# Kernel optimization log

Hardware: AMD Instinct MI355X
Metric: run time of the kernel (lower is better)

The kernel has to match this reference:

```python
import jax, jax.numpy as jnp
import numpy as np

B, S, D, H = 4, 2048, 1024, 16
HD = D // H
BITS = 8
LEVELS = 2 ** BITS - 1          # number of negative log2 levels
SCALING = 32.0 / 16.0           # lora alpha / rank for 8-bit adapter
NEG_INF = -1e9


def log_fake_quant(x, reduce_axes):
    """Per-channel log-domain fake quantization with straight-through estimator.
    Scale = per-channel max-abs; magnitudes snapped to power-of-two fractions of scale."""
    s = jnp.maximum(jnp.max(jnp.abs(x), axis=reduce_axes, keepdims=True), 1e-8)
    ratio = jnp.clip(jnp.abs(x) / s, 2.0 ** (-LEVELS), 1.0)
    e = jnp.round(jnp.log2(ratio))                      # in [-LEVELS, 0]
    q = jnp.sign(x) * s * jnp.exp2(e)
    return x + jax.lax.stop_gradient(q - x)             # STE


def cpt_linear(x, W, b, lA, lB):
    """CPTLinear: fake-quantized activation/weight GEMM + bias + LoRA on the fp input."""
    xq = log_fake_quant(x, tuple(range(x.ndim - 1)))     # per last-dim channel
    Wq = log_fake_quant(W, (1,))                         # per output row (channel_dim=0)
    out = xq @ Wq.T + b
    return out + (x @ lA @ lB) * SCALING


def setup_inputs() -> dict:
    key = jax.random.key(0)
    ks = jax.random.split(key, 8)
    causal = jnp.tril(jnp.ones((S, S), dtype=bool))
    mask = jnp.where(causal, 0.0, NEG_INF).astype(jnp.float32)[None, None]  # [1,1,S,S]
    return {
        "hidden_states": jax.random.normal(ks[0], (B, S, D), jnp.float32),
        "attention_mask": mask,
        "W_attn": jax.random.normal(ks[1], (3 * D, D), jnp.float32) * 0.02,
        "b_attn": jnp.zeros((3 * D,), jnp.float32),
        "lA_attn": jax.random.normal(ks[2], (D, 16), jnp.float32) * 0.01,
        "lB_attn": jax.random.normal(ks[3], (16, 3 * D), jnp.float32) * 0.01,
        "W_proj": jax.random.normal(ks[4], (D, D), jnp.float32) * 0.02,
        "b_proj": jnp.zeros((D,), jnp.float32),
        "lA_proj": jax.random.normal(ks[5], (D, 16), jnp.float32) * 0.01,
        "lB_proj": jax.random.normal(ks[6], (16, D), jnp.float32) * 0.01,
    }


def reference(hidden_states, attention_mask, W_attn, b_attn, lA_attn, lB_attn,
              W_proj, b_proj, lA_proj, lB_proj):
    qkv = cpt_linear(hidden_states, W_attn, b_attn, lA_attn, lB_attn)  # [B,S,3D]
    q, k, v = jnp.split(qkv, 3, axis=-1)

    def to_heads(t):
        return t.reshape(B, S, H, HD).transpose(0, 2, 1, 3)            # [B,H,S,HD]

    q, k, v = to_heads(q), to_heads(k), to_heads(v)
    scores = jnp.einsum("bhqd,bhkd->bhqk", q, k) / np.float32(np.sqrt(HD))
    scores = scores + attention_mask
    attn = jax.nn.softmax(scores, axis=-1)                             # dropout: eval mode (identity)
    out = jnp.einsum("bhqk,bhkd->bhqd", attn, v)
    out = out.transpose(0, 2, 1, 3).reshape(B, S, D)
    return cpt_linear(out, W_proj, b_proj, lA_proj, lB_proj)
```

## Files before the change

kernel.cpp:

```cpp
#include <hip/hip_runtime.h>

#define SS 2048
#define DD 1024
#define DQKV 3072
#define KP 1088
#define NT64 17
#define MTOT 8192
#define QKSZ ((size_t)MTOT * DD)
#define SCL 0.18033688011112042f

typedef unsigned short us;
typedef __attribute__((ext_vector_type(8))) short bf16x8;
typedef __attribute__((ext_vector_type(4))) float f32x4;
typedef __attribute__((ext_vector_type(4))) unsigned u32x4;

#define WAITVM(N) asm volatile("s_waitcnt vmcnt(" #N ")" ::: "memory")
#define WAITLGKM0 asm volatile("s_waitcnt lgkmcnt(0)" ::: "memory")

__device__ __forceinline__ us f2bf(float f) {
    unsigned u = __float_as_uint(f);
    return (us)((u + 0x7fffu + ((u >> 16) & 1u)) >> 16);
}
__device__ __forceinline__ float bf2f(us h) { return __uint_as_float(((unsigned)h) << 16); }
__device__ __forceinline__ void split2(float q, us& h, us& l) {
    h = f2bf(q); l = f2bf(q - bf2f(h));
}
__device__ __forceinline__ unsigned cvtpk(float lo, float hi) {
    unsigned r;
    asm("v_cvt_pk_bf16_f32 %0, %1, %2" : "=v"(r) : "v"(lo), "v"(hi));
    return r;
}

__device__ __forceinline__ int logq_e(float ax, float s) {
    int e = 0;
    if (ax < s) {
        int ex;
        float m = frexpf(ax / s, &ex);
        int k = (m >= 0.70710678f) ? ex : ex - 1;
        double ax2 = (double)ax * (double)ax;
        double s2 = (double)s * (double)s;
        if (ax2 >= ldexp(s2, 2 * k + 1)) k += 1;
        else if (ax2 < ldexp(s2, 2 * k - 1)) k -= 1;
        if (k > 0) k = 0;
        e = (k < -255) ? -255 : k;
    }
    return e;
}
__device__ __forceinline__ float logq_exact(float x, float s) {
    float ax = fabsf(x);
    if (ax == 0.f) return copysignf(0.f, x);
    return copysignf(ldexpf(s, logq_e(ax, s)), x);
}

__device__ __forceinline__ void gll16(const void* g, void* l) {
    __builtin_amdgcn_global_load_lds(
        (const __attribute__((address_space(1))) void*)g,
        (__attribute__((address_space(3))) void*)l, 16, 0, 0);
}


__global__ void k_colmax(const float* __restrict__ x, unsigned* __restrict__ smax) {
    int c = blockIdx.x * 256 + threadIdx.x;
    int r0 = blockIdx.y * 128;
    float m = 0.f;
    for (int r = 0; r < 128; ++r) m = fmaxf(m, fabsf(x[(size_t)(r0 + r) * DD + c]));
    atomicMax(smax + c, __float_as_uint(m));
}

__global__ __launch_bounds__(256) void k_quant_lora(const float* __restrict__ x,
                                                    const unsigned* __restrict__ smax,
                                                    const float* __restrict__ lA,
                                                    us* __restrict__ xq) {
    __shared__ float red[4][16];
    int m = blockIdx.x, tx = threadIdx.x;
    int lane = tx & 63, w = tx >> 6;
    float4 xv = ((const float4*)(x + (size_t)m * DD))[tx];
    int c = tx * 4;
    float vv[4] = {xv.x, xv.y, xv.z, xv.w};
    ushort4 qh;
    us* ph = (us*)&qh;
#pragma unroll
    for (int j = 0; j < 4; ++j) {
        float s = fmaxf(__uint_as_float(smax[c + j]), 1e-8f);
        float sh = bf2f(f2bf(s));
        float ax = fabsf(vv[j]);
        if (ax == 0.f) ph[j] = (us)((__float_as_uint(vv[j]) >> 16) & 0x8000u);
        else ph[j] = f2bf(copysignf(ldexpf(sh, logq_e(ax, s)), vv[j]));
    }
    *(ushort4*)(xq + (size_t)m * KP + c) = qh;
    float acc[16];
#pragma unroll
    for (int r = 0; r < 16; ++r) acc[r] = 0.f;
#pragma unroll
    for (int j = 0; j < 4; ++j) {
        float xs = vv[j];
        const float4* lr = (const float4*)(lA + (size_t)(c + j) * 16);
        float4 a0 = lr[0], a1 = lr[1], a2 = lr[2], a3 = lr[3];
        acc[0] += xs * a0.x; acc[1] += xs * a0.y; acc[2] += xs * a0.z; acc[3] += xs * a0.w;
        acc[4] += xs * a1.x; acc[5] += xs * a1.y; acc[6] += xs * a1.z; acc[7] += xs * a1.w;
        acc[8] += xs * a2.x; acc[9] += xs * a2.y; acc[10] += xs * a2.z; acc[11] += xs * a2.w;
        acc[12] += xs * a3.x; acc[13] += xs * a3.y; acc[14] += xs * a3.z; acc[15] += xs * a3.w;
    }
#pragma unroll
    for (int msk = 1; msk < 64; msk <<= 1)
#pragma unroll
        for (int r = 0; r < 16; ++r) acc[r] += __shfl_xor(acc[r], msk);
    if (lane == 0)
#pragma unroll
        for (int r = 0; r < 16; ++r) red[w][r] = acc[r];
    __syncthreads();
    if (tx < 16) {
        float v = 2.0f * (red[0][tx] + red[1][tx] + red[2][tx] + red[3][tx]);
        us h, l; split2(v, h, l);
        xq[(size_t)m * KP + 1024 + tx] = h;
        xq[(size_t)m * KP + 1040 + tx] = l;
    } else if (tx == 16) {
        xq[(size_t)m * KP + 1056] = 0x3F80;
    } else if (tx < 48) {
        xq[(size_t)m * KP + 1040 + tx] = 0;
    }
}

__global__ __launch_bounds__(256) void k_quant_w(const float* __restrict__ W, const float* __restrict__ lB,
                                                 const float* __restrict__ bias,
                                                 const unsigned* __restrict__ smax,
                                                 us* __restrict__ wh, us* __restrict__ wl, int Nn) {
    __shared__ float red[4];
    int n = blockIdx.x, tx = threadIdx.x;
    int lane = tx & 63, w = tx >> 6;
    float4 wv = ((const float4*)(W + (size_t)n * DD))[tx];
    float m4 = fmaxf(fmaxf(fabsf(wv.x), fabsf(wv.y)), fmaxf(fabsf(wv.z), fabsf(wv.w)));
#pragma unroll
    for (int msk = 1; msk < 64; msk <<= 1) m4 = fmaxf(m4, __shfl_xor(m4, msk));
    if (lane == 0) red[w] = m4;
    __syncthreads();
    float t = fmaxf(fmaxf(fmaxf(red[0], red[1]), fmaxf(red[2], red[3])), 1e-8f);
    float vv[4] = {wv.x, wv.y, wv.z, wv.w};
    int c = tx * 4;
    ushort4 qh, ql;
    us* ph = (us*)&qh; us* pl = (us*)&ql;
#pragma unroll
    for (int j = 0; j < 4; ++j) {
        float s = fmaxf(__uint_as_float(smax[c + j]), 1e-8f);
        float sh = bf2f(f2bf(s));
        float rho = (s - sh) / sh;
        float q = logq_exact(vv[j], t);
        float wp = q + q * rho;
        split2(wp, ph[j], pl[j]);
    }
    *(ushort4*)(wh + (size_t)n * KP + c) = qh;
    *(ushort4*)(wl + (size_t)n * KP + c) = ql;
    if (tx < 64) {
        us h = 0, l = 0;
        if (tx < 32) { int r = tx & 15; split2(lB[(size_t)r * Nn + n], h, l); }
        else if (tx == 32) split2(bias[n], h, l);
        wh[(size_t)n * KP + 1024 + tx] = h;
        wl[(size_t)n * KP + 1024 + tx] = l;
    }
}


template <int MODE>
__global__ __launch_bounds__(512, 2) void k_gemm(const us* __restrict__ Aq_,
                                                 const us* __restrict__ Bh_, const us* __restrict__ Bl_,
                                                 float* __restrict__ C, int Nn,
                                                 us* __restrict__ Khg, us* __restrict__ Klg,
                                                 float* __restrict__ vbuf) {
    __shared__ us LA[2][16384];
    __shared__ us LBh[2][8192];
    __shared__ us LBl[2][8192];
    int tid = threadIdx.x;
    int bn = blockIdx.x, bm = blockIdx.y;
    int lane = tid & 63, w = tid >> 6;
    int wm = w >> 2, wn = w & 3;
    int l15 = lane & 15, l4 = lane >> 4;
    int srow = tid >> 3;
    int gsrc = ((tid & 7) ^ (srow & 7)) * 8;
    const us* aP  = Aq_ + (size_t)(bm * 256 + srow) * KP + gsrc;
    const us* bhP = Bh_ + (size_t)(bn * 128 + srow) * KP + gsrc;
    const us* blP = Bl_ + (size_t)(bn * 128 + srow) * KP + gsrc;
    f32x4 zero4 = {0.f, 0.f, 0.f, 0.f};
    f32x4 acc[8][2];
#pragma unroll
    for (int i = 0; i < 8; ++i) { acc[i][0] = zero4; acc[i][1] = zero4; }

#define GSTAGE(buf, kt)                                               \
    do {                                                              \
        int k0_ = (kt) * 64;                                          \
        gll16(aP + k0_,                    &LA[(buf)][0]     + tid * 8); \
        gll16(aP + (size_t)64  * KP + k0_, &LA[(buf)][4096]  + tid * 8); \
        gll16(aP + (size_t)128 * KP + k0_, &LA[(buf)][8192]  + tid * 8); \
        gll16(aP + (size_t)192 * KP + k0_, &LA[(buf)][12288] + tid * 8); \
        gll16(bhP + k0_,                   &LBh[(buf)][0]    + tid * 8); \
        gll16(bhP + (size_t)64 * KP + k0_, &LBh[(buf)][4096] + tid * 8); \
        gll16(blP + k0_,                   &LBl[(buf)][0]    + tid * 8); \
        gll16(blP + (size_t)64 * KP + k0_, &LBl[(buf)][4096] + tid * 8); \
    } while (0)

    GSTAGE(0, 0);
    GSTAGE(1, 1);
    WAITVM(8);
    __builtin_amdgcn_s_barrier();
    __builtin_amdgcn_sched_barrier(0);

    int gsw0 = ((l4)     ^ (l15 & 7)) * 8;
    int gsw1 = ((4 + l4) ^ (l15 & 7)) * 8;
    int cur = 0;
    for (int kt = 0; kt < NT64; ++kt) {
        const us* A0  = &LA[cur][0];
        const us* Bh0 = &LBh[cur][0];
        const us* Bl0 = &LBl[cur][0];
        bf16x8 a0[8], b0h[2], b0l[2];
#pragma unroll
        for (int i = 0; i < 8; ++i)
            a0[i] = *(const bf16x8*)(A0 + (wm * 128 + i * 16 + l15) * 64 + gsw0);
#pragma unroll
        for (int i = 0; i < 2; ++i) {
            b0h[i] = *(const bf16x8*)(Bh0 + (wn * 32 + i * 16 + l15) * 64 + gsw0);
            b0l[i] = *(const bf16x8*)(Bl0 + (wn * 32 + i * 16 + l15) * 64 + gsw0);
        }
        __builtin_amdgcn_s_setprio(1);
#pragma unroll
        for (int mi = 0; mi < 8; ++mi)
#pragma unroll
            for (int ni = 0; ni < 2; ++ni) {
                acc[mi][ni] = __builtin_amdgcn_mfma_f32_16x16x32_bf16(a0[mi], b0h[ni], acc[mi][ni], 0, 0, 0);
                acc[mi][ni] = __builtin_amdgcn_mfma_f32_16x16x32_bf16(a0[mi], b0l[ni], acc[mi][ni], 0, 0, 0);
            }
        __builtin_amdgcn_s_setprio(0);
        bf16x8 a1[8], b1h[2], b1l[2];
#pragma unroll
        for (int i = 0; i < 8; ++i)
            a1[i] = *(const bf16x8*)(A0 + (wm * 128 + i * 16 + l15) * 64 + gsw1);
#pragma unroll
        for (int i = 0; i < 2; ++i) {
            b1h[i] = *(const bf16x8*)(Bh0 + (wn * 32 + i * 16 + l15) * 64 + gsw1);
            b1l[i] = *(const bf16x8*)(Bl0 + (wn * 32 + i * 16 + l15) * 64 + gsw1);
        }
        WAITLGKM0;
        __builtin_amdgcn_sched_barrier(0);
        __builtin_amdgcn_s_barrier();
        __builtin_amdgcn_sched_barrier(0);
        if (kt + 2 < NT64) GSTAGE(cur, kt + 2);
        __builtin_amdgcn_s_setprio(1);
#pragma unroll
        for (int mi = 0; mi < 8; ++mi)
#pragma unroll
            for (int ni = 0; ni < 2; ++ni) {
                acc[mi][ni] = __builtin_amdgcn_mfma_f32_16x16x32_bf16(a1[mi], b1h[ni], acc[mi][ni], 0, 0, 0);
                acc[mi][ni] = __builtin_amdgcn_mfma_f32_16x16x32_bf16(a1[mi], b1l[ni], acc[mi][ni], 0, 0, 0);
            }
        __builtin_amdgcn_s_setprio(0);
        if (kt + 2 < NT64) { WAITVM(8); } else { WAITVM(0); }
        __builtin_amdgcn_s_barrier();
        __builtin_amdgcn_sched_barrier(0);
        cur ^= 1;
    }
#undef GSTAGE

    int plane = bn >> 3;
#pragma unroll
    for (int mi = 0; mi < 8; ++mi) {
#pragma unroll
        for (int ni = 0; ni < 2; ++ni) {
            int ncol = bn * 128 + wn * 32 + ni * 16 + l15;
            size_t mbase = (size_t)bm * 256 + wm * 128 + mi * 16 + l4 * 4;
#pragma unroll
            for (int rr = 0; rr < 4; ++rr) {
                float v = acc[mi][ni][rr];
                size_t m = mbase + rr;
                if (MODE == 0) {
                    C[m * (size_t)Nn + ncol] = v;
                } else {
                    int cc = ncol & 1023;
                    if (plane == 0) {
                        C[m * DD + cc] = v;
                    } else if (plane == 2) {
                        vbuf[m * DD + cc] = v;
                    } else {
                        us hh, ll; split2(v * SCL, hh, ll);
                        size_t d = ((size_t)((m >> 11) * 16 + (cc >> 6)) * SS + (m & 2047)) * 64 + (cc & 63);
                        Khg[d] = hh; Klg[d] = ll;
                    }
                }
            }
        }
    }
}


__global__ __launch_bounds__(256) void k_transpose_v(const float* __restrict__ vbuf,
                                                     us* __restrict__ vth, us* __restrict__ vtl) {
    __shared__ us th[64][72], tl[64][72];
    int st = blockIdx.x, bh = blockIdx.y;
    int bb = bh >> 4, h = bh & 15;
    int s0 = st * 64, tid = threadIdx.x;
    int sl = tid >> 2, c0 = (tid & 3) * 16;
    const float* src = vbuf + (size_t)(bb * SS + s0 + sl) * DD + h * 64 + c0;
#pragma unroll
    for (int j4 = 0; j4 < 4; ++j4) {
        float4 v = *(const float4*)(src + j4 * 4);
        float vv[4] = {v.x, v.y, v.z, v.w};
#pragma unroll
        for (int j = 0; j < 4; ++j) {
            us hh, ll; split2(vv[j], hh, ll);
            th[c0 + j4 * 4 + j][sl] = hh;
            tl[c0 + j4 * 4 + j][sl] = ll;
        }
    }
    __syncthreads();
#pragma unroll
    for (int p = 0; p < 2; ++p) {
        int gidx = p * 256 + tid;
        int hd = gidx >> 3, g = gidx & 7;
        int base = (g >> 2) * 32 + (g & 3) * 4;
        ushort4 a, b2, c, d2;
        a.x = th[hd][base];      a.y = th[hd][base + 1];  a.z = th[hd][base + 2];  a.w = th[hd][base + 3];
        b2.x = th[hd][base + 16]; b2.y = th[hd][base + 17]; b2.z = th[hd][base + 18]; b2.w = th[hd][base + 19];
        c.x = tl[hd][base];      c.y = tl[hd][base + 1];  c.z = tl[hd][base + 2];  c.w = tl[hd][base + 3];
        d2.x = tl[hd][base + 16]; d2.y = tl[hd][base + 17]; d2.z = tl[hd][base + 18]; d2.w = tl[hd][base + 19];
        size_t dof = ((size_t)bh * 64 + hd) * SS + s0 + g * 8;
        *(ushort4*)(vth + dof) = a;  *(ushort4*)(vth + dof + 4) = b2;
        *(ushort4*)(vtl + dof) = c;  *(ushort4*)(vtl + dof + 4) = d2;
    }
}


__global__ __launch_bounds__(512, 2) void k_attn(float* qo,
                                                 const us* __restrict__ Khg, const us* __restrict__ Klg,
                                                 const us* __restrict__ vth, const us* __restrict__ vtl) {
    __shared__ us L[2][16384];
    int bh = blockIdx.x;
    int qt = (int)(gridDim.y - 1) - blockIdx.y;
    int b = bh >> 4, h = bh & 15;
    int q0 = qt * 128;
    int tid = threadIdx.x, w = tid >> 6, lane = tid & 63;
    int l15 = lane & 15, l4 = lane >> 4;
    int qw = q0 + w * 16;
    int swz = l15 & 7;

    bf16x8 qh[2], ql[2];
#pragma unroll
    for (int hf = 0; hf < 2; ++hf) {
        const float* qp = qo + (size_t)(b * SS + qw + l15) * DD + h * 64 + hf * 32 + l4 * 8;
        float4 a = *(const float4*)qp;
        float4 c = *(const float4*)(qp + 4);
        float vv[8] = {a.x, a.y, a.z, a.w, c.x, c.y, c.z, c.w};
        bf16x8 hq, lq;
#pragma unroll
        for (int j = 0; j < 8; ++j) {
            us hh = f2bf(vv[j]);
            hq[j] = (short)hh;
            lq[j] = (short)f2bf(vv[j] - bf2f(hh));
        }
        qh[hf] = hq; ql[hf] = lq;
    }

    f32x4 zero4 = {0.f, 0.f, 0.f, 0.f};
    f32x4 of[4];
#pragma unroll
    for (int j = 0; j < 4; ++j) of[j] = zero4;
    float mrow = -1e30f, lrowp = 0.f;

    int r0 = tid >> 3, sl0 = (tid & 7) ^ (r0 & 7);
    int koff0 = (bh * SS + r0) * 64 + sl0 * 8;
    int voff0 = (bh * 64 + r0) * SS + sl0 * 8;

    int ntiles = qt * 2 + 2;

#define STAGE(buf, tt)                                           \
    do {                                                         \
        int kv_ = (tt) * 64;                                     \
        us* D_ = &L[(buf)][0];                                   \
        int kadd_ = kv_ << 6;                                    \
        gll16(Khg + koff0 + kadd_, D_ + tid * 8);                \
        gll16(Klg + koff0 + kadd_, D_ + 4096 + tid * 8);         \
        gll16(vth + voff0 + kv_, D_ + 8192 + tid * 8);           \
        gll16(vtl + voff0 + kv_, D_ + 12288 + tid * 8);          \
    } while (0)

    STAGE(0, 0);
    STAGE(1, 1);
    int cur = 0;

    for (int t = 0; t < ntiles; ++t) {
        int kv0 = t * 64;
        if (t + 1 < ntiles) { WAITVM(4); } else { WAITVM(0); }
        __builtin_amdgcn_s_barrier();

        if (kv0 <= qw + 15) {
            const us* Lc = &L[cur][0];

            f32x4 sf[4];
#pragma unroll
            for (int i = 0; i < 4; ++i) sf[i] = zero4;
            __builtin_amdgcn_s_setprio(1);
#pragma unroll
            for (int kb = 0; kb < 4; ++kb) {
                int rbase = (kb * 16 + l15) * 64;
#pragma unroll
                for (int hf = 0; hf < 2; ++hf) {
                    int off = rbase + (((hf * 4 + l4) ^ swz) * 8);
                    bf16x8 kh = *(const bf16x8*)(Lc + off);
                    bf16x8 kl = *(const bf16x8*)(Lc + 4096 + off);
                    sf[kb] = __builtin_amdgcn_mfma_f32_16x16x32_bf16(kh, qh[hf], sf[kb], 0, 0, 0);
                    sf[kb] = __builtin_amdgcn_mfma_f32_16x16x32_bf16(kh, ql[hf], sf[kb], 0, 0, 0);
                    sf[kb] = __builtin_amdgcn_mfma_f32_16x16x32_bf16(kl, qh[hf], sf[kb], 0, 0, 0);
                }
            }
            __builtin_amdgcn_s_setprio(0);

            bool diag = (kv0 + 63 > qw);
            u32x4 PH[2], PL[2];
            {
                float pv[16];
                if (diag) {
                    int qg = qw + l15;
#pragma unroll
                    for (int kb = 0; kb < 4; ++kb)
#pragma unroll
                        for (int rr = 0; rr < 4; ++rr) {
                            int kvg = kv0 + kb * 16 + l4 * 4 + rr;
                            pv[kb * 4 + rr] = (kvg > qg) ? -1e30f : sf[kb][rr];
                        }
                } else {
#pragma unroll
                    for (int kb = 0; kb < 4; ++kb)
#pragma unroll
                        for (int rr = 0; rr < 4; ++rr)
                            pv[kb * 4 + rr] = sf[kb][rr];
                }
                float t0 = fmaxf(fmaxf(pv[0], pv[1]), pv[2]);
                float t1 = fmaxf(fmaxf(pv[3], pv[4]), pv[5]);
                float t2 = fmaxf(fmaxf(pv[6], pv[7]), pv[8]);
                float t3 = fmaxf(fmaxf(pv[9], pv[10]), pv[11]);
                float t4 = fmaxf(fmaxf(pv[12], pv[13]), pv[14]);
                float tmax = fmaxf(fmaxf(fmaxf(t0, t1), fmaxf(t2, t3)), fmaxf(t4, pv[15]));
                tmax = fmaxf(tmax, __shfl_xor(tmax, 16));
                tmax = fmaxf(tmax, __shfl_xor(tmax, 32));
                float mcur = mrow;
                if (!__all(tmax <= mcur + 8.0f)) {
                    float mnew = fmaxf(mcur, tmax);
                    float fac = __builtin_amdgcn_exp2f(mcur - mnew);
                    mrow = mnew; mcur = mnew;
                    lrowp *= fac;
                    float fr0 = __shfl(fac, l4 * 4 + 0);
                    float fr1 = __shfl(fac, l4 * 4 + 1);
                    float fr2 = __shfl(fac, l4 * 4 + 2);
                    float fr3 = __shfl(fac, l4 * 4 + 3);
#pragma unroll
                    for (int hb = 0; hb < 4; ++hb) {
                        of[hb][0] *= fr0; of[hb][1] *= fr1;
                        of[hb][2] *= fr2; of[hb][3] *= fr3;
                    }
                }
                float ps = 0.f;
#pragma unroll
                for (int i = 0; i < 16; ++i) {
                    pv[i] = __builtin_amdgcn_exp2f(pv[i] - mcur);
                    ps += pv[i];
                }
                lrowp += ps;
#pragma unroll
                for (int ks = 0; ks < 2; ++ks)
#pragma unroll
                    for (int c2 = 0; c2 < 4; ++c2) {
                        float p0 = pv[ks * 8 + c2 * 2], p1 = pv[ks * 8 + c2 * 2 + 1];
                        unsigned u = cvtpk(p0, p1);
                        float h0 = __uint_as_float(u << 16);
                        float h1 = __uint_as_float(u & 0xffff0000u);
                        unsigned ul = cvtpk(p0 - h0, p1 - h1);
                        PH[ks][c2] = u; PL[ks][c2] = ul;
                    }
            }

            __builtin_amdgcn_s_setprio(1);
#pragma unroll
            for (int hb = 0; hb < 4; ++hb) {
                int rbase = (hb * 16 + l15) * 64;
#pragma unroll
                for (int ks = 0; ks < 2; ++ks) {
                    int off = rbase + (((ks * 4 + l4) ^ swz) * 8);
                    bf16x8 vh = *(const bf16x8*)(Lc + 8192 + off);
                    bf16x8 vl = *(const bf16x8*)(Lc + 12288 + off);
                    bf16x8 pa = (bf16x8)PH[ks];
                    bf16x8 pb = (bf16x8)PL[ks];
                    of[hb] = __builtin_amdgcn_mfma_f32_16x16x32_bf16(pa, vh, of[hb], 0, 0, 0);
                    of[hb] = __builtin_amdgcn_mfma_f32_16x16x32_bf16(pa, vl, of[hb], 0, 0, 0);
                    of[hb] = __builtin_amdgcn_mfma_f32_16x16x32_bf16(pb, vh, of[hb], 0, 0, 0);
                }
            }
            __builtin_amdgcn_s_setprio(0);
        }

        __builtin_amdgcn_s_barrier();
        if (t + 2 < ntiles) STAGE(cur, t + 2);
        cur ^= 1;
    }
#undef STAGE

    {
        float lr = lrowp;
        lr += __shfl_xor(lr, 16);
        lr += __shfl_xor(lr, 32);
        float linv = 1.f / lr;
        float f0 = __shfl(linv, l4 * 4 + 0);
        float f1 = __shfl(linv, l4 * 4 + 1);
        float f2 = __shfl(linv, l4 * 4 + 2);
        float f3 = __shfl(linv, l4 * 4 + 3);
        int qgb = qw + l4 * 4;
#pragma unroll
        for (int hb = 0; hb < 4; ++hb) {
            int col = h * 64 + hb * 16 + l15;
            qo[((size_t)(b * SS + qgb + 0)) * DD + col] = of[hb][0] * f0;
            qo[((size_t)(b * SS + qgb + 1)) * DD + col] = of[hb][1] * f1;
            qo[((size_t)(b * SS + qgb + 2)) * DD + col] = of[hb][2] * f2;
            qo[((size_t)(b * SS + qgb + 3)) * DD + col] = of[hb][3] * f3;
        }
    }
}


extern "C" void kernel_launch(void* const* d_in, const int* in_sizes, int n_in,
                              void* d_out, int out_size, void* d_ws, size_t ws_size,
                              hipStream_t stream) {
    const float* hidden  = (const float*)d_in[0];
    const float* W_attn  = (const float*)d_in[2];
    const float* b_attn  = (const float*)d_in[3];
    const float* lA_attn = (const float*)d_in[4];
    const float* lB_attn = (const float*)d_in[5];
    const float* W_proj  = (const float*)d_in[6];
    const float* b_proj  = (const float*)d_in[7];
    const float* lA_proj = (const float*)d_in[8];
    const float* lB_proj = (const float*)d_in[9];
    float* out = (float*)d_out;

    char* ws = (char*)d_ws;
    unsigned* s1 = (unsigned*)(ws);
    unsigned* s2 = (unsigned*)(ws + 4096);
    us* xq  = (us*)(ws + 8192);
    us* vth = xq;
    us* wh1 = (us*)(ws + 8192 + 17825792);
    us* wl1 = (us*)(ws + 8192 + 17825792 + 6684672);
    us* wh2 = (us*)(ws + 8192 + 17825792 + 2 * 6684672);
    us* wl2 = (us*)(ws + 8192 + 17825792 + 2 * 6684672 + 2228224);
    char* pbase = ws + 8192 + 17825792 + 2 * 6684672 + 2 * 2228224;
    float* qbuf = (float*)pbase;
    float* vbuf = (float*)(pbase + 33554432);
    us* Khg = (us*)(pbase + 2 * (size_t)33554432);
    us* Klg = (us*)(pbase + 2 * (size_t)33554432 + 16777216);
    us* vtl = (us*)(pbase + 2 * (size_t)33554432 + 2 * (size_t)16777216);

    hipMemsetAsync(ws, 0, 8192, stream);

    k_colmax<<<dim3(4, 64), 256, 0, stream>>>(hidden, s1);
    k_quant_lora<<<MTOT, 256, 0, stream>>>(hidden, s1, lA_attn, xq);
    k_quant_w<<<3072, 256, 0, stream>>>(W_attn, lB_attn, b_attn, s1, wh1, wl1, 3072);
    k_gemm<1><<<dim3(24, 32), 512, 0, stream>>>(xq, wh1, wl1, qbuf, DQKV, Khg, Klg, vbuf);

    k_transpose_v<<<dim3(32, 64), 256, 0, stream>>>(vbuf, vth, vtl);
    k_attn<<<dim3(64, 16), 512, 0, stream>>>(qbuf, Khg, Klg, vth, vtl);

    k_colmax<<<dim3(4, 64), 256, 0, stream>>>(qbuf, s2);
    k_quant_lora<<<MTOT, 256, 0, stream>>>(qbuf, s2, lA_proj, xq);
    k_quant_w<<<1024, 256, 0, stream>>>(W_proj, lB_proj, b_proj, s2, wh2, wl2, 1024);
    k_gemm<0><<<dim3(8, 32), 512, 0, stream>>>(xq, wh2, wl2, out, DD, nullptr, nullptr, nullptr);
}
```

Before: 455.7 us.

## Fuse V transpose and bf16 split into QKV GEMM epilogue; swap grid order

The QKV GEMM epilogue now splits V values into hi/lo bf16 and writes them straight into the transposed layout the attention kernel reads. This removes the fp32 V buffer round trip and the separate transpose kernel launch. The grid is also reordered so the M tile is blockIdx.x, which changes which blocks run together and how weight and activation tiles are reused in L2. The epilogue stores for V are now scattered 8-byte writes along the sequence dimension, which may coalesce poorly.

```diff
diff --git a/kernel.cpp b/kernel.cpp
--- a/kernel.cpp
+++ b/kernel.cpp
@@ -165,12 +165,12 @@
                                                  const us* __restrict__ Bh_, const us* __restrict__ Bl_,
                                                  float* __restrict__ C, int Nn,
                                                  us* __restrict__ Khg, us* __restrict__ Klg,
-                                                 float* __restrict__ vbuf) {
+                                                 us* __restrict__ vth, us* __restrict__ vtl) {
     __shared__ us LA[2][16384];
     __shared__ us LBh[2][8192];
     __shared__ us LBl[2][8192];
     int tid = threadIdx.x;
-    int bn = blockIdx.x, bm = blockIdx.y;
+    int bm = blockIdx.x, bn = blockIdx.y;
     int lane = tid & 63, w = tid >> 6;
     int wm = w >> 2, wn = w & 3;
     int l15 = lane & 15, l4 = lane >> 4;
@@ -265,63 +265,40 @@
         for (int ni = 0; ni < 2; ++ni) {
             int ncol = bn * 128 + wn * 32 + ni * 16 + l15;
             size_t mbase = (size_t)bm * 256 + wm * 128 + mi * 16 + l4 * 4;
-#pragma unroll
-            for (int rr = 0; rr < 4; ++rr) {
-                float v = acc[mi][ni][rr];
-                size_t m = mbase + rr;
-                if (MODE == 0) {
-                    C[m * (size_t)Nn + ncol] = v;
-                } else {
-                    int cc = ncol & 1023;
-                    if (plane == 0) {
-                        C[m * DD + cc] = v;
-                    } else if (plane == 2) {
-                        vbuf[m * DD + cc] = v;
-                    } else {
-                        us hh, ll; split2(v * SCL, hh, ll);
+            if (MODE == 0) {
+#pragma unroll
+                for (int rr = 0; rr < 4; ++rr)
+                    C[(mbase + rr) * (size_t)Nn + ncol] = acc[mi][ni][rr];
+            } else {
+                int cc = ncol & 1023;
+                if (plane == 0) {
+#pragma unroll
+                    for (int rr = 0; rr < 4; ++rr)
+                        C[(mbase + rr) * DD + cc] = acc[mi][ni][rr];
+                } else if (plane == 1) {
+#pragma unroll
+                    for (int rr = 0; rr < 4; ++rr) {
+                        size_t m = mbase + rr;
+                        us hh, ll; split2(acc[mi][ni][rr] * SCL, hh, ll);
                         size_t d = ((size_t)((m >> 11) * 16 + (cc >> 6)) * SS + (m & 2047)) * 64 + (cc & 63);
                         Khg[d] = hh; Klg[d] = ll;
                     }
+                } else {
+                    int bq = (int)(mbase >> 11), sq = (int)(mbase & 2047);
+                    int chunk = sq >> 6, s6 = sq & 63;
+                    int g = ((s6 >> 5) << 2) | ((s6 >> 2) & 3);
+                    int j = ((s6 >> 4) & 1) << 2;
+                    size_t dof = ((size_t)((bq << 4) + (cc >> 6)) * 64 + (cc & 63)) * SS
+                               + (chunk << 6) + (g << 3) + j;
+                    ushort4 vh4, vl4;
+                    us* hp = (us*)&vh4; us* lp = (us*)&vl4;
+#pragma unroll
+                    for (int rr = 0; rr < 4; ++rr) split2(acc[mi][ni][rr], hp[rr], lp[rr]);
+                    *(ushort4*)(vth + dof) = vh4;
+                    *(ushort4*)(vtl + dof) = vl4;
                 }
             }
         }
-    }
-}
-
-
-__global__ __launch_bounds__(256) void k_transpose_v(const float* __restrict__ vbuf,
-                                                     us* __restrict__ vth, us* __restrict__ vtl) {
-    __shared__ us th[64][72], tl[64][72];
-    int st = blockIdx.x, bh = blockIdx.y;
-    int bb = bh >> 4, h = bh & 15;
-    int s0 = st * 64, tid = threadIdx.x;
-    int sl = tid >> 2, c0 = (tid & 3) * 16;
-    const float* src = vbuf + (size_t)(bb * SS + s0 + sl) * DD + h * 64 + c0;
-#pragma unroll
-    for (int j4 = 0; j4 < 4; ++j4) {
-        float4 v = *(const float4*)(src + j4 * 4);
-        float vv[4] = {v.x, v.y, v.z, v.w};
-#pragma unroll
-        for (int j = 0; j < 4; ++j) {
-            us hh, ll; split2(vv[j], hh, ll);
-            th[c0 + j4 * 4 + j][sl] = hh;
-            tl[c0 + j4 * 4 + j][sl] = ll;
-        }
-    }
-    __syncthreads();
-#pragma unroll
-    for (int p = 0; p < 2; ++p) {
-        int gidx = p * 256 + tid;
-        int hd = gidx >> 3, g = gidx & 7;
-        int base = (g >> 2) * 32 + (g & 3) * 4;
-        ushort4 a, b2, c, d2;
-        a.x = th[hd][base];      a.y = th[hd][base + 1];  a.z = th[hd][base + 2];  a.w = th[hd][base + 3];
-        b2.x = th[hd][base + 16]; b2.y = th[hd][base + 17]; b2.z = th[hd][base + 18]; b2.w = th[hd][base + 19];
-        c.x = tl[hd][base];      c.y = tl[hd][base + 1];  c.z = tl[hd][base + 2];  c.w = tl[hd][base + 3];
-        d2.x = tl[hd][base + 16]; d2.y = tl[hd][base + 17]; d2.z = tl[hd][base + 18]; d2.w = tl[hd][base + 19];
-        size_t dof = ((size_t)bh * 64 + hd) * SS + s0 + g * 8;
-        *(ushort4*)(vth + dof) = a;  *(ushort4*)(vth + dof + 4) = b2;
-        *(ushort4*)(vtl + dof) = c;  *(ushort4*)(vtl + dof + 4) = d2;
     }
 }
 
@@ -539,30 +516,28 @@
     unsigned* s1 = (unsigned*)(ws);
     unsigned* s2 = (unsigned*)(ws + 4096);
     us* xq  = (us*)(ws + 8192);
-    us* vth = xq;
     us* wh1 = (us*)(ws + 8192 + 17825792);
     us* wl1 = (us*)(ws + 8192 + 17825792 + 6684672);
     us* wh2 = (us*)(ws + 8192 + 17825792 + 2 * 6684672);
     us* wl2 = (us*)(ws + 8192 + 17825792 + 2 * 6684672 + 2228224);
     char* pbase = ws + 8192 + 17825792 + 2 * 6684672 + 2 * 2228224;
     float* qbuf = (float*)pbase;
-    float* vbuf = (float*)(pbase + 33554432);
-    us* Khg = (us*)(pbase + 2 * (size_t)33554432);
-    us* Klg = (us*)(pbase + 2 * (size_t)33554432 + 16777216);
-    us* vtl = (us*)(pbase + 2 * (size_t)33554432 + 2 * (size_t)16777216);
+    us* vth = (us*)(pbase + 33554432);
+    us* vtl = (us*)(pbase + 33554432 + 16777216);
+    us* Khg = (us*)(pbase + 33554432 + 2 * (size_t)16777216);
+    us* Klg = (us*)(pbase + 33554432 + 3 * (size_t)16777216);
 
     hipMemsetAsync(ws, 0, 8192, stream);
 
     k_colmax<<<dim3(4, 64), 256, 0, stream>>>(hidden, s1);
     k_quant_lora<<<MTOT, 256, 0, stream>>>(hidden, s1, lA_attn, xq);
     k_quant_w<<<3072, 256, 0, stream>>>(W_attn, lB_attn, b_attn, s1, wh1, wl1, 3072);
-    k_gemm<1><<<dim3(24, 32), 512, 0, stream>>>(xq, wh1, wl1, qbuf, DQKV, Khg, Klg, vbuf);
-
-    k_transpose_v<<<dim3(32, 64), 256, 0, stream>>>(vbuf, vth, vtl);
+    k_gemm<1><<<dim3(32, 24), 512, 0, stream>>>(xq, wh1, wl1, qbuf, DQKV, Khg, Klg, vth, vtl);
+
     k_attn<<<dim3(64, 16), 512, 0, stream>>>(qbuf, Khg, Klg, vth, vtl);
 
     k_colmax<<<dim3(4, 64), 256, 0, stream>>>(qbuf, s2);
     k_quant_lora<<<MTOT, 256, 0, stream>>>(qbuf, s2, lA_proj, xq);
     k_quant_w<<<1024, 256, 0, stream>>>(W_proj, lB_proj, b_proj, s2, wh2, wl2, 1024);
-    k_gemm<0><<<dim3(8, 32), 512, 0, stream>>>(xq, wh2, wl2, out, DD, nullptr, nullptr, nullptr);
-}
+    k_gemm<0><<<dim3(32, 8), 512, 0, stream>>>(xq, wh2, wl2, out, DD, nullptr, nullptr, nullptr, nullptr);
+}
```

Result: faster. 439.5 us, median of 2 (-3.6%).
